# Performance work log

Hardware: AMD Instinct MI355X
Metric: run time of the kernel (lower is better)

## Reference

```python
import jax, jax.numpy as jnp
import numpy as np
from jax import lax

CHUNK = 256  # points of the query set processed per step; intermediate is [B, CHUNK, M]


def _nn_min(x, y):
    """For each point in x [B,N,3], squared distance + index of nearest point in y [B,M,3].
    Chunked over N so the full [B,N,M] distance matrix is never materialized."""
    B, N, _ = x.shape
    y2 = jnp.sum(y * y, axis=-1)  # [B, M]
    K = N // CHUNK
    xr = jnp.swapaxes(x.reshape(B, K, CHUNK, 3), 0, 1)  # [K, B, CHUNK, 3]

    def chunk_fn(xc):  # xc: [B, CHUNK, 3]
        d = (jnp.sum(xc * xc, axis=-1)[..., None]
             - 2.0 * jnp.einsum('bcd,bmd->bcm', xc, y)
             + y2[:, None, :])  # [B, CHUNK, M]
        return jnp.min(d, axis=-1), jnp.argmin(d, axis=-1).astype(jnp.int32)

    dmin, idx = lax.map(chunk_fn, xr)  # [K, B, CHUNK]
    dmin = jnp.swapaxes(dmin, 0, 1).reshape(B, N)
    idx = jnp.swapaxes(idx, 0, 1).reshape(B, N)
    return dmin, idx


def setup_inputs() -> dict:
    key = jax.random.key(0)
    k1, k2 = jax.random.split(key)
    xyz1 = jax.random.normal(k1, (8, 16384, 3), dtype=jnp.float32)
    xyz2 = jax.random.normal(k2, (8, 16384, 3), dtype=jnp.float32)
    return {"xyz1": xyz1, "xyz2": xyz2}


def reference(xyz1, xyz2):
    dist1, idx1 = _nn_min(xyz1, xyz2)  # [B, N], [B, N]
    dist2, idx2 = _nn_min(xyz2, xyz1)  # [B, M], [B, M]
    return dist1, dist2, idx1, idx2
```

## Files before the change

kernel.cpp:

```cpp
#include <hip/hip_runtime.h>
#include <stdint.h>

#define BATCH 8
#define NPTS  16384
#define BN    (BATCH * NPTS)
#define CH    256
#define NCH   (NPTS / CH)
#define QPB   256
#define MARGIN 4.0e-3f

typedef float f32x16 __attribute__((ext_vector_type(16)));
typedef short s16x8  __attribute__((ext_vector_type(8)));

__device__ __forceinline__ uint16_t bfr(float x) {
    uint32_t u = __float_as_uint(x);
    return (uint16_t)((u + 0x7FFFu + ((u >> 16) & 1u)) >> 16);
}
__device__ __forceinline__ float bff(uint16_t s) {
    return __uint_as_float(((uint32_t)s) << 16);
}
__device__ __forceinline__ void split2(float v, uint16_t* a, uint16_t* b) {
    *a = bfr(v); *b = bfr(v - bff(*a));
}
__device__ __forceinline__ uint32_t pk2(uint16_t lo, uint16_t hi) {
    return (uint32_t)lo | ((uint32_t)hi << 16);
}
__device__ __forceinline__ uint32_t key32(float d) {
    uint32_t b = __float_as_uint(d);
    return (b & 0x80000000u) ? ~b : (b | 0x80000000u);
}
__device__ __forceinline__ float dec32(uint32_t k) {
    return __uint_as_float((k & 0x80000000u) ? (k ^ 0x80000000u) : ~k);
}

#define F16(M_) M_(0) M_(1) M_(2) M_(3) M_(4) M_(5) M_(6) M_(7) \
                M_(8) M_(9) M_(10) M_(11) M_(12) M_(13) M_(14) M_(15)

#define MIN3(a, b, c) fminf(fminf((a), (b)), (c))

__device__ __forceinline__ float fold16(const f32x16 a) {
    const float u0 = MIN3(a[0],  a[1],  a[2]);
    const float u1 = MIN3(a[3],  a[4],  a[5]);
    const float u2 = MIN3(a[6],  a[7],  a[8]);
    const float u3 = MIN3(a[9],  a[10], a[11]);
    const float u4 = MIN3(a[12], a[13], a[14]);
    const float v0 = MIN3(u0, u1, a[15]);
    const float v1 = MIN3(u2, u3, u4);
    return fminf(v0, v1);
}

__global__ __launch_bounds__(256) void enc_kernel(
    const float* __restrict__ Y, uint4* __restrict__ enc,
    float4* __restrict__ y4)
{
#pragma clang fp contract(off)
    const int g = blockIdx.x * 256 + threadIdx.x;
    const int b = g >> 14, p = g & (NPTS - 1);
    const float y0 = Y[(size_t)g * 3 + 0];
    const float y1 = Y[(size_t)g * 3 + 1];
    const float y2 = Y[(size_t)g * 3 + 2];
    const float ys = (y0 * y0 + y1 * y1) + y2 * y2;
    uint16_t Ya, Yb; split2(ys, &Ya, &Yb);
    uint16_t H0, M0; split2(-2.0f * y0, &H0, &M0);
    uint16_t H1, M1; split2(-2.0f * y1, &H1, &M1);
    uint16_t H2, M2; split2(-2.0f * y2, &H2, &M2);
    const uint16_t ONE = 0x3F80;
    const int ch = p >> 8, pp = p & (CH - 1);
    const size_t base = (size_t)(b * NCH + ch) * (2 * CH) + pp;
    enc[base]      = make_uint4(pk2(ONE, ONE), pk2(Ya, Yb), pk2(H0, M0), pk2(H0, M0));
    enc[base + CH] = make_uint4(pk2(H1, M1), pk2(H1, M1), pk2(H2, M2), pk2(H2, M2));
    y4[g] = make_float4(y0, y1, y2, ys);
}

#define DECODE_DBX() \
    int dir, batch, kh, xblk; \
    { const int g = blockIdx.x; \
      if (ndir == 2) { const int s = 2 * (g & 7) + ((g >> 3) & 1); \
          dir = s >> 3; batch = s & 7; kh = (g >> 4) & 1; xblk = g >> 5; } \
      else { dir = dir0; batch = g & 7; kh = (g >> 3) & 1; xblk = g >> 4; } }

#define STAGE(c, buf) { \
        const uint4* src_ = ep + (size_t)(c) * (2 * CH); \
        _Pragma("unroll") \
        for (int i_ = 0; i_ < 2; ++i_) \
            __builtin_amdgcn_global_load_lds( \
                (const __attribute__((address_space(1))) void*)(src_ + i_ * 256 + tid), \
                (__attribute__((address_space(3))) void*)&lds[buf][i_ * 256 + tid], \
                16, 0, 0); \
    }

#define MKQFR(dst, qq, qx0v, qx1v, qx2v, qxsv) { \
        const float* xp = Xp + (size_t)(bofs + (qq)) * 3; \
        qx0v = xp[0]; qx1v = xp[1]; qx2v = xp[2]; \
        qxsv = (qx0v * qx0v + qx1v * qx1v) + qx2v * qx2v; \
        uint16_t Xa, Xb; split2(qxsv, &Xa, &Xb); \
        uint16_t h0, m0; split2(qx0v, &h0, &m0); \
        uint16_t h1, m1; split2(qx1v, &h1, &m1); \
        uint16_t h2, m2; split2(qx2v, &h2, &m2); \
        const uint16_t ONE = 0x3F80; \
        if (hi == 0) { \
            dst[0]=(short)Xa; dst[1]=(short)Xb; dst[2]=(short)ONE; dst[3]=(short)ONE; \
            dst[4]=(short)h0; dst[5]=(short)h0; dst[6]=(short)m0;  dst[7]=(short)m0; \
        } else { \
            dst[0]=(short)h1; dst[1]=(short)h1; dst[2]=(short)m1;  dst[3]=(short)m1; \
            dst[4]=(short)h2; dst[5]=(short)h2; dst[6]=(short)m2;  dst[7]=(short)m2; \
        } }

__global__ __launch_bounds__(256, 4) void nn_fused(
    const float* __restrict__ xyz1, const float* __restrict__ xyz2,
    const uint4* __restrict__ encA, const uint4* __restrict__ encB,
    const float4* __restrict__ y4A, const float4* __restrict__ y4B,
    unsigned long long* __restrict__ gkeys, int ndir, int dir0)
{
#pragma clang fp contract(off)
    __shared__ uint4 lds[2][2 * CH];
    __shared__ unsigned long long keys[QPB];

    const int tid = threadIdx.x;
    const int l   = tid & 63;
    const int wv  = tid >> 6;
    const int col = l & 31;
    const int hi  = l >> 5;
    DECODE_DBX()

    const float*  Xp = dir ? xyz2 : xyz1;
    const uint4*  ep = (dir ? encB : encA) + (size_t)batch * (NCH * 2 * CH);
    const float4* Y4 = (dir ? y4B : y4A) + (size_t)batch * NPTS;
    const int bofs  = batch * NPTS;
    const int qbase = xblk * QPB + wv * 64;
    const int chalf = NCH / 2;
    const int c0 = kh * chalf, c1 = c0 + chalf;

    keys[tid] = ~0ull;

    const f32x16 zf = {0.f,0.f,0.f,0.f,0.f,0.f,0.f,0.f,
                       0.f,0.f,0.f,0.f,0.f,0.f,0.f,0.f};

    int rowpack[4] = {0, 0, 0, 0};
    {
        s16x8 pa = {0,0,0,0,0,0,0,0}, pb = {0,0,0,0,0,0,0,0};
        if (hi == 0) { pa[0] = (short)bfr((float)col); pb[0] = (short)0x3F80; }
        const f32x16 rowp = __builtin_amdgcn_mfma_f32_32x32x16_bf16(pa, pb, zf, 0, 0, 0);
#define PR(i) rowpack[(i) >> 2] |= ((int)rowp[i] & 0xFF) << (((i) & 3) * 8);
        F16(PR)
#undef PR
    }

    s16x8 qfr0, qfr1;
    float qa0, qa1, qa2, qas, qb0, qb1, qb2, qbs;
    MKQFR(qfr0, qbase + col,      qa0, qa1, qa2, qas)
    MKQFR(qfr1, qbase + 32 + col, qb0, qb1, qb2, qbs)

    const int ldsb = hi * CH + col;

    float run0 = __builtin_inff(), run1 = __builtin_inff();

    STAGE(c0, 0);
    __syncthreads();
#pragma unroll
    for (int tp = 0; tp < CH / 32; ++tp) {
        const s16x8 pA = *(const s16x8*)&lds[0][ldsb + tp * 32];
        const f32x16 a0 = __builtin_amdgcn_mfma_f32_32x32x16_bf16(pA, qfr0, zf, 0, 0, 0);
        run0 = fminf(run0, fold16(a0));
        const f32x16 a1 = __builtin_amdgcn_mfma_f32_32x32x16_bf16(pA, qfr1, zf, 0, 0, 0);
        run1 = fminf(run1, fold16(a1));
    }
    run0 = fminf(run0, __shfl_xor(run0, 32, 64));
    run1 = fminf(run1, __shfl_xor(run1, 32, 64));

#define HITR(accv, jb, foff, thr, qx0, qx1, qx2, qxs, r) \
        if ((accv)[r] <= (thr)) { \
            const int jc = (jb) + ((rowpack[(r) >> 2] >> (((r) & 3) * 8)) & 0xFF); \
            const float4 yv = Y4[jc]; \
            const float dd = ((qxs) - 2.0f * (((qx0) * yv.x + (qx1) * yv.y) + (qx2) * yv.z)) + yv.w; \
            atomicMin(&keys[wv * 64 + (foff) + col], \
                      ((unsigned long long)key32(dd) << 32) | (uint32_t)jc); }
#define HIT(accv, jb, foff, thr, qx0, qx1, qx2, qxs) \
        { \
            HITR(accv, jb, foff, thr, qx0, qx1, qx2, qxs, 0) \
            HITR(accv, jb, foff, thr, qx0, qx1, qx2, qxs, 1) \
            HITR(accv, jb, foff, thr, qx0, qx1, qx2, qxs, 2) \
            HITR(accv, jb, foff, thr, qx0, qx1, qx2, qxs, 3) \
            HITR(accv, jb, foff, thr, qx0, qx1, qx2, qxs, 4) \
            HITR(accv, jb, foff, thr, qx0, qx1, qx2, qxs, 5) \
            HITR(accv, jb, foff, thr, qx0, qx1, qx2, qxs, 6) \
            HITR(accv, jb, foff, thr, qx0, qx1, qx2, qxs, 7) \
            HITR(accv, jb, foff, thr, qx0, qx1, qx2, qxs, 8) \
            HITR(accv, jb, foff, thr, qx0, qx1, qx2, qxs, 9) \
            HITR(accv, jb, foff, thr, qx0, qx1, qx2, qxs, 10) \
            HITR(accv, jb, foff, thr, qx0, qx1, qx2, qxs, 11) \
            HITR(accv, jb, foff, thr, qx0, qx1, qx2, qxs, 12) \
            HITR(accv, jb, foff, thr, qx0, qx1, qx2, qxs, 13) \
            HITR(accv, jb, foff, thr, qx0, qx1, qx2, qxs, 14) \
            HITR(accv, jb, foff, thr, qx0, qx1, qx2, qxs, 15) \
        }

    int cur = 0;
    for (int c = c0; c < c1; ++c) {
        if (c + 1 < c1) STAGE(c + 1, cur ^ 1);
#pragma unroll
        for (int tp = 0; tp < CH / 32; ++tp) {
            const s16x8 pA = *(const s16x8*)&lds[cur][ldsb + tp * 32];
            const int jb = c * CH + tp * 32;
            {
                const f32x16 a0 = __builtin_amdgcn_mfma_f32_32x32x16_bf16(pA, qfr0, zf, 0, 0, 0);
                const float f0 = fold16(a0);
                run0 = fminf(run0, f0);
                const float t0v = run0 + MARGIN;
                if (f0 <= t0v) HIT(a0, jb, 0, t0v, qa0, qa1, qa2, qas)
            }
            {
                const f32x16 a1 = __builtin_amdgcn_mfma_f32_32x32x16_bf16(pA, qfr1, zf, 0, 0, 0);
                const float f1 = fold16(a1);
                run1 = fminf(run1, f1);
                const float t1v = run1 + MARGIN;
                if (f1 <= t1v) HIT(a1, jb, 32, t1v, qb0, qb1, qb2, qbs)
            }
        }
        run0 = fminf(run0, __shfl_xor(run0, 32, 64));
        run1 = fminf(run1, __shfl_xor(run1, 32, 64));
        __syncthreads();
        cur ^= 1;
    }
#undef HIT
#undef HITR

    __syncthreads();
    {
        const unsigned long long m = keys[tid];
        const size_t gq = (size_t)dir * BN + bofs + (size_t)xblk * QPB + tid;
        atomicMin(&gkeys[gq], m);
    }
}

__global__ __launch_bounds__(256) void writeout_k(
    const unsigned long long* __restrict__ gkeys, float* __restrict__ out)
{
    const size_t i = (size_t)blockIdx.x * 256 + threadIdx.x;
    const unsigned long long m = gkeys[i];
    const int dir = (int)(i / BN);
    const size_t q = i - (size_t)dir * BN;
    out[(size_t)dir * BN + q]       = dec32((uint32_t)(m >> 32));
    out[(size_t)(2 + dir) * BN + q] = (float)(uint32_t)(m & 0xFFFFFFFFu);
}

extern "C" void kernel_launch(void* const* d_in, const int* in_sizes, int n_in,
                              void* d_out, int out_size, void* d_ws, size_t ws_size,
                              hipStream_t stream) {
    const float* xyz1 = (const float*)d_in[0];
    const float* xyz2 = (const float*)d_in[1];
    float* out = (float*)d_out;

    if (ws_size >= (size_t)15 * 1024 * 1024) {
        uint4*  encA = (uint4*)d_ws;
        uint4*  encB = encA + (size_t)2 * BN;
        float4* y4A  = (float4*)(encB + (size_t)2 * BN);
        float4* y4B  = y4A + BN;
        unsigned long long* gkeys = (unsigned long long*)(y4B + BN);

        enc_kernel<<<BN / 256, 256, 0, stream>>>(xyz2, encA, y4A);
        enc_kernel<<<BN / 256, 256, 0, stream>>>(xyz1, encB, y4B);
        hipMemsetAsync(gkeys, 0xFF, (size_t)2 * 1024 * 1024, stream);
        nn_fused<<<2048, 256, 0, stream>>>(xyz1, xyz2, encA, encB, y4A, y4B,
                                           gkeys, 2, 0);
        writeout_k<<<(2 * BN) / 256, 256, 0, stream>>>(gkeys, out);
    } else {
        uint4*  enc = (uint4*)d_ws;
        float4* y4  = (float4*)(enc + (size_t)2 * BN);
        unsigned long long* gkeys = (unsigned long long*)(y4 + BN);

        hipMemsetAsync(gkeys, 0xFF, (size_t)2 * 1024 * 1024, stream);
        enc_kernel<<<BN / 256, 256, 0, stream>>>(xyz2, enc, y4);
        nn_fused<<<1024, 256, 0, stream>>>(xyz1, xyz2, enc, enc, y4, y4,
                                           gkeys, 1, 0);
        enc_kernel<<<BN / 256, 256, 0, stream>>>(xyz1, enc, y4);
        nn_fused<<<1024, 256, 0, stream>>>(xyz1, xyz2, enc, enc, y4, y4,
                                           gkeys, 1, 1);
        writeout_k<<<(2 * BN) / 256, 256, 0, stream>>>(gkeys, out);
    }
}
```

Before: 413.8 us.

## Split NN search into MFMA chunk-min sweep, flagging, and exact candidate walk

Replaces the fused kernel, which checked hits inline, with a multi-pass pipeline. First an MFMA sweep records a bf16 per-chunk minimum for every query (chunk size doubled to 512) along with a global running minimum. A flag kernel then queues the chunks whose minimum lies within a margin of the best. Finally a walk kernel does exact fp32 distance evaluation over only the queued chunks, one wave per entry. This removes divergent per-element hit handling and LDS atomics from the hot MFMA loop. In exchange it adds extra launches, memsets, processes the two directions serially, tightens the margin, and caps the queue, so overflow could drop candidates.

```diff
diff --git a/kernel.cpp b/kernel.cpp
--- a/kernel.cpp
+++ b/kernel.cpp
@@ -4,10 +4,11 @@
 #define BATCH 8
 #define NPTS  16384
 #define BN    (BATCH * NPTS)
-#define CH    256
+#define CH    512
 #define NCH   (NPTS / CH)
 #define QPB   256
-#define MARGIN 4.0e-3f
+#define MARGIN 3.0e-3f
+#define QCAP  (1u << 20)
 
 typedef float f32x16 __attribute__((ext_vector_type(16)));
 typedef short s16x8  __attribute__((ext_vector_type(8)));
@@ -32,9 +33,6 @@
 __device__ __forceinline__ float dec32(uint32_t k) {
     return __uint_as_float((k & 0x80000000u) ? (k ^ 0x80000000u) : ~k);
 }
-
-#define F16(M_) M_(0) M_(1) M_(2) M_(3) M_(4) M_(5) M_(6) M_(7) \
-                M_(8) M_(9) M_(10) M_(11) M_(12) M_(13) M_(14) M_(15)
 
 #define MIN3(a, b, c) fminf(fminf((a), (b)), (c))
 
@@ -65,38 +63,31 @@
     uint16_t H1, M1; split2(-2.0f * y1, &H1, &M1);
     uint16_t H2, M2; split2(-2.0f * y2, &H2, &M2);
     const uint16_t ONE = 0x3F80;
-    const int ch = p >> 8, pp = p & (CH - 1);
+    const int ch = p >> 9, pp = p & (CH - 1);
     const size_t base = (size_t)(b * NCH + ch) * (2 * CH) + pp;
     enc[base]      = make_uint4(pk2(ONE, ONE), pk2(Ya, Yb), pk2(H0, M0), pk2(H0, M0));
     enc[base + CH] = make_uint4(pk2(H1, M1), pk2(H1, M1), pk2(H2, M2), pk2(H2, M2));
     y4[g] = make_float4(y0, y1, y2, ys);
 }
 
-#define DECODE_DBX() \
-    int dir, batch, kh, xblk; \
-    { const int g = blockIdx.x; \
-      if (ndir == 2) { const int s = 2 * (g & 7) + ((g >> 3) & 1); \
-          dir = s >> 3; batch = s & 7; kh = (g >> 4) & 1; xblk = g >> 5; } \
-      else { dir = dir0; batch = g & 7; kh = (g >> 3) & 1; xblk = g >> 4; } }
-
 #define STAGE(c, buf) { \
         const uint4* src_ = ep + (size_t)(c) * (2 * CH); \
         _Pragma("unroll") \
-        for (int i_ = 0; i_ < 2; ++i_) \
+        for (int i_ = 0; i_ < 4; ++i_) \
             __builtin_amdgcn_global_load_lds( \
                 (const __attribute__((address_space(1))) void*)(src_ + i_ * 256 + tid), \
                 (__attribute__((address_space(3))) void*)&lds[buf][i_ * 256 + tid], \
                 16, 0, 0); \
     }
 
-#define MKQFR(dst, qq, qx0v, qx1v, qx2v, qxsv) { \
-        const float* xp = Xp + (size_t)(bofs + (qq)) * 3; \
-        qx0v = xp[0]; qx1v = xp[1]; qx2v = xp[2]; \
-        qxsv = (qx0v * qx0v + qx1v * qx1v) + qx2v * qx2v; \
-        uint16_t Xa, Xb; split2(qxsv, &Xa, &Xb); \
-        uint16_t h0, m0; split2(qx0v, &h0, &m0); \
-        uint16_t h1, m1; split2(qx1v, &h1, &m1); \
-        uint16_t h2, m2; split2(qx2v, &h2, &m2); \
+#define MKQFR(dst, qq) { \
+        const float* xp = Xp + (size_t)(qq) * 3; \
+        const float x0 = xp[0], x1 = xp[1], x2 = xp[2]; \
+        const float xs = (x0 * x0 + x1 * x1) + x2 * x2; \
+        uint16_t Xa, Xb; split2(xs, &Xa, &Xb); \
+        uint16_t h0, m0; split2(x0, &h0, &m0); \
+        uint16_t h1, m1; split2(x1, &h1, &m1); \
+        uint16_t h2, m2; split2(x2, &h2, &m2); \
         const uint16_t ONE = 0x3F80; \
         if (hi == 0) { \
             dst[0]=(short)Xa; dst[1]=(short)Xb; dst[2]=(short)ONE; dst[3]=(short)ONE; \
@@ -106,140 +97,146 @@
             dst[4]=(short)h2; dst[5]=(short)h2; dst[6]=(short)m2;  dst[7]=(short)m2; \
         } }
 
-__global__ __launch_bounds__(256, 4) void nn_fused(
-    const float* __restrict__ xyz1, const float* __restrict__ xyz2,
-    const uint4* __restrict__ encA, const uint4* __restrict__ encB,
-    const float4* __restrict__ y4A, const float4* __restrict__ y4B,
-    unsigned long long* __restrict__ gkeys, int ndir, int dir0)
+__global__ __launch_bounds__(256, 4) void nn_sweep1(
+    const float* __restrict__ Xp, const uint4* __restrict__ encp,
+    uint32_t* __restrict__ mkey, uint16_t* __restrict__ cmin16)
 {
 #pragma clang fp contract(off)
     __shared__ uint4 lds[2][2 * CH];
-    __shared__ unsigned long long keys[QPB];
 
     const int tid = threadIdx.x;
     const int l   = tid & 63;
     const int wv  = tid >> 6;
     const int col = l & 31;
     const int hi  = l >> 5;
-    DECODE_DBX()
-
-    const float*  Xp = dir ? xyz2 : xyz1;
-    const uint4*  ep = (dir ? encB : encA) + (size_t)batch * (NCH * 2 * CH);
-    const float4* Y4 = (dir ? y4B : y4A) + (size_t)batch * NPTS;
+
+    const int g     = blockIdx.x;
+    const int batch = g & 7;
+    const int kh    = (g >> 3) & 1;
+    const int xblk  = g >> 4;
+
+    const uint4* ep = encp + (size_t)batch * (NCH * 2 * CH);
     const int bofs  = batch * NPTS;
-    const int qbase = xblk * QPB + wv * 64;
-    const int chalf = NCH / 2;
-    const int c0 = kh * chalf, c1 = c0 + chalf;
-
-    keys[tid] = ~0ull;
+    const int qbase = bofs + xblk * QPB + wv * 64;
+    const int c0 = kh * (NCH / 2), c1 = c0 + NCH / 2;
 
     const f32x16 zf = {0.f,0.f,0.f,0.f,0.f,0.f,0.f,0.f,
                        0.f,0.f,0.f,0.f,0.f,0.f,0.f,0.f};
 
-    int rowpack[4] = {0, 0, 0, 0};
-    {
-        s16x8 pa = {0,0,0,0,0,0,0,0}, pb = {0,0,0,0,0,0,0,0};
-        if (hi == 0) { pa[0] = (short)bfr((float)col); pb[0] = (short)0x3F80; }
-        const f32x16 rowp = __builtin_amdgcn_mfma_f32_32x32x16_bf16(pa, pb, zf, 0, 0, 0);
-#define PR(i) rowpack[(i) >> 2] |= ((int)rowp[i] & 0xFF) << (((i) & 3) * 8);
-        F16(PR)
-#undef PR
-    }
-
     s16x8 qfr0, qfr1;
-    float qa0, qa1, qa2, qas, qb0, qb1, qb2, qbs;
-    MKQFR(qfr0, qbase + col,      qa0, qa1, qa2, qas)
-    MKQFR(qfr1, qbase + 32 + col, qb0, qb1, qb2, qbs)
+    MKQFR(qfr0, qbase + col)
+    MKQFR(qfr1, qbase + 32 + col)
 
     const int ldsb = hi * CH + col;
 
     float run0 = __builtin_inff(), run1 = __builtin_inff();
-
     STAGE(c0, 0);
     __syncthreads();
-#pragma unroll
-    for (int tp = 0; tp < CH / 32; ++tp) {
-        const s16x8 pA = *(const s16x8*)&lds[0][ldsb + tp * 32];
-        const f32x16 a0 = __builtin_amdgcn_mfma_f32_32x32x16_bf16(pA, qfr0, zf, 0, 0, 0);
-        run0 = fminf(run0, fold16(a0));
-        const f32x16 a1 = __builtin_amdgcn_mfma_f32_32x32x16_bf16(pA, qfr1, zf, 0, 0, 0);
-        run1 = fminf(run1, fold16(a1));
-    }
-    run0 = fminf(run0, __shfl_xor(run0, 32, 64));
-    run1 = fminf(run1, __shfl_xor(run1, 32, 64));
-
-#define HITR(accv, jb, foff, thr, qx0, qx1, qx2, qxs, r) \
-        if ((accv)[r] <= (thr)) { \
-            const int jc = (jb) + ((rowpack[(r) >> 2] >> (((r) & 3) * 8)) & 0xFF); \
-            const float4 yv = Y4[jc]; \
-            const float dd = ((qxs) - 2.0f * (((qx0) * yv.x + (qx1) * yv.y) + (qx2) * yv.z)) + yv.w; \
-            atomicMin(&keys[wv * 64 + (foff) + col], \
-                      ((unsigned long long)key32(dd) << 32) | (uint32_t)jc); }
-#define HIT(accv, jb, foff, thr, qx0, qx1, qx2, qxs) \
-        { \
-            HITR(accv, jb, foff, thr, qx0, qx1, qx2, qxs, 0) \
-            HITR(accv, jb, foff, thr, qx0, qx1, qx2, qxs, 1) \
-            HITR(accv, jb, foff, thr, qx0, qx1, qx2, qxs, 2) \
-            HITR(accv, jb, foff, thr, qx0, qx1, qx2, qxs, 3) \
-            HITR(accv, jb, foff, thr, qx0, qx1, qx2, qxs, 4) \
-            HITR(accv, jb, foff, thr, qx0, qx1, qx2, qxs, 5) \
-            HITR(accv, jb, foff, thr, qx0, qx1, qx2, qxs, 6) \
-            HITR(accv, jb, foff, thr, qx0, qx1, qx2, qxs, 7) \
-            HITR(accv, jb, foff, thr, qx0, qx1, qx2, qxs, 8) \
-            HITR(accv, jb, foff, thr, qx0, qx1, qx2, qxs, 9) \
-            HITR(accv, jb, foff, thr, qx0, qx1, qx2, qxs, 10) \
-            HITR(accv, jb, foff, thr, qx0, qx1, qx2, qxs, 11) \
-            HITR(accv, jb, foff, thr, qx0, qx1, qx2, qxs, 12) \
-            HITR(accv, jb, foff, thr, qx0, qx1, qx2, qxs, 13) \
-            HITR(accv, jb, foff, thr, qx0, qx1, qx2, qxs, 14) \
-            HITR(accv, jb, foff, thr, qx0, qx1, qx2, qxs, 15) \
-        }
-
     int cur = 0;
     for (int c = c0; c < c1; ++c) {
         if (c + 1 < c1) STAGE(c + 1, cur ^ 1);
+        float cm0 = __builtin_inff(), cm1 = __builtin_inff();
 #pragma unroll
         for (int tp = 0; tp < CH / 32; ++tp) {
             const s16x8 pA = *(const s16x8*)&lds[cur][ldsb + tp * 32];
-            const int jb = c * CH + tp * 32;
-            {
-                const f32x16 a0 = __builtin_amdgcn_mfma_f32_32x32x16_bf16(pA, qfr0, zf, 0, 0, 0);
-                const float f0 = fold16(a0);
-                run0 = fminf(run0, f0);
-                const float t0v = run0 + MARGIN;
-                if (f0 <= t0v) HIT(a0, jb, 0, t0v, qa0, qa1, qa2, qas)
-            }
-            {
-                const f32x16 a1 = __builtin_amdgcn_mfma_f32_32x32x16_bf16(pA, qfr1, zf, 0, 0, 0);
-                const float f1 = fold16(a1);
-                run1 = fminf(run1, f1);
-                const float t1v = run1 + MARGIN;
-                if (f1 <= t1v) HIT(a1, jb, 32, t1v, qb0, qb1, qb2, qbs)
-            }
-        }
-        run0 = fminf(run0, __shfl_xor(run0, 32, 64));
-        run1 = fminf(run1, __shfl_xor(run1, 32, 64));
+            const f32x16 a0 = __builtin_amdgcn_mfma_f32_32x32x16_bf16(pA, qfr0, zf, 0, 0, 0);
+            cm0 = fminf(cm0, fold16(a0));
+            const f32x16 a1 = __builtin_amdgcn_mfma_f32_32x32x16_bf16(pA, qfr1, zf, 0, 0, 0);
+            cm1 = fminf(cm1, fold16(a1));
+        }
+        cm0 = fminf(cm0, __shfl_xor(cm0, 32, 64));
+        cm1 = fminf(cm1, __shfl_xor(cm1, 32, 64));
+        run0 = fminf(run0, cm0);
+        run1 = fminf(run1, cm1);
+        if (l < 32) {
+            cmin16[(size_t)(qbase + col) * NCH + c]      =
+                (uint16_t)(__float_as_uint(cm0) >> 16);
+            cmin16[(size_t)(qbase + 32 + col) * NCH + c] =
+                (uint16_t)(__float_as_uint(cm1) >> 16);
+        }
         __syncthreads();
         cur ^= 1;
     }
-#undef HIT
-#undef HITR
-
-    __syncthreads();
-    {
-        const unsigned long long m = keys[tid];
-        const size_t gq = (size_t)dir * BN + bofs + (size_t)xblk * QPB + tid;
-        atomicMin(&gkeys[gq], m);
+    if (l < 32) {
+        atomicMin(&mkey[qbase + col],      key32(run0));
+        atomicMin(&mkey[qbase + 32 + col], key32(run1));
+    }
+}
+
+__global__ __launch_bounds__(256) void flag_kernel(
+    const uint32_t* __restrict__ mkey, const uint16_t* __restrict__ cmin16,
+    uint32_t* __restrict__ queue, uint32_t* __restrict__ qcount)
+{
+    const int q = blockIdx.x * 256 + threadIdx.x;
+    const float thr = dec32(mkey[q]) + MARGIN + 1.0e-5f;
+    const uint4* row = (const uint4*)(cmin16 + (size_t)q * NCH);
+    uint32_t fl = 0;
+#pragma unroll
+    for (int w = 0; w < 4; ++w) {
+        const uint4 u = row[w];
+        const uint32_t c[4] = {u.x, u.y, u.z, u.w};
+#pragma unroll
+        for (int j = 0; j < 4; ++j) {
+            if (bff((uint16_t)(c[j] & 0xFFFF)) <= thr) fl |= 1u << (w * 8 + j * 2);
+            if (bff((uint16_t)(c[j] >> 16))    <= thr) fl |= 1u << (w * 8 + j * 2 + 1);
+        }
+    }
+    const int nfl = __popc(fl);
+    uint32_t base = atomicAdd(qcount, (uint32_t)nfl);
+    while (fl) {
+        const int ch = __ffs(fl) - 1;
+        fl &= fl - 1;
+        if (base < QCAP) queue[base] = ((uint32_t)q << 5) | (uint32_t)ch;
+        ++base;
+    }
+}
+
+__global__ __launch_bounds__(256, 8) void walk_kernel(
+    const float* __restrict__ Xp, const float4* __restrict__ y4,
+    const uint32_t* __restrict__ queue, const uint32_t* __restrict__ qcount,
+    unsigned long long* __restrict__ gkeys)
+{
+#pragma clang fp contract(off)
+    const int lane = threadIdx.x & 63;
+    const uint32_t wid = blockIdx.x * 4 + (threadIdx.x >> 6);
+    const uint32_t nw  = gridDim.x * 4;
+    const uint32_t cnt = min(*qcount, QCAP);
+
+    for (uint32_t e = wid; e < cnt; e += nw) {
+        const uint32_t entry = queue[e];
+        const int q  = (int)(entry >> 5);
+        const int ch = (int)(entry & 31);
+        const int b  = q >> 14;
+
+        const float* xp = Xp + (size_t)q * 3;
+        const float qx0 = xp[0], qx1 = xp[1], qx2 = xp[2];
+        const float qxs = (qx0 * qx0 + qx1 * qx1) + qx2 * qx2;
+
+        const float4* yb = y4 + (size_t)b * NPTS + (size_t)ch * CH;
+        unsigned long long best = ~0ull;
+#pragma unroll
+        for (int j = 0; j < CH / 64; ++j) {
+            const int k = j * 64 + lane;
+            const float4 yv = yb[k];
+            const float dd = (qxs - 2.0f * ((qx0 * yv.x + qx1 * yv.y) + qx2 * yv.z)) + yv.w;
+            const unsigned long long key =
+                ((unsigned long long)key32(dd) << 32) | (uint32_t)(ch * CH + k);
+            if (key < best) best = key;
+        }
+#pragma unroll
+        for (int m = 1; m <= 32; m <<= 1) {
+            const unsigned long long o = __shfl_xor(best, m, 64);
+            if (o < best) best = o;
+        }
+        if (lane == 0) atomicMin(&gkeys[q], best);
     }
 }
 
 __global__ __launch_bounds__(256) void writeout_k(
-    const unsigned long long* __restrict__ gkeys, float* __restrict__ out)
-{
-    const size_t i = (size_t)blockIdx.x * 256 + threadIdx.x;
-    const unsigned long long m = gkeys[i];
-    const int dir = (int)(i / BN);
-    const size_t q = i - (size_t)dir * BN;
+    const unsigned long long* __restrict__ gkeys, float* __restrict__ out, int dir)
+{
+    const size_t q = (size_t)blockIdx.x * 256 + threadIdx.x;
+    const unsigned long long m = gkeys[q];
     out[(size_t)dir * BN + q]       = dec32((uint32_t)(m >> 32));
     out[(size_t)(2 + dir) * BN + q] = (float)(uint32_t)(m & 0xFFFFFFFFu);
 }
@@ -251,31 +248,28 @@
     const float* xyz2 = (const float*)d_in[1];
     float* out = (float*)d_out;
 
-    if (ws_size >= (size_t)15 * 1024 * 1024) {
-        uint4*  encA = (uint4*)d_ws;
-        uint4*  encB = encA + (size_t)2 * BN;
-        float4* y4A  = (float4*)(encB + (size_t)2 * BN);
-        float4* y4B  = y4A + BN;
-        unsigned long long* gkeys = (unsigned long long*)(y4B + BN);
-
-        enc_kernel<<<BN / 256, 256, 0, stream>>>(xyz2, encA, y4A);
-        enc_kernel<<<BN / 256, 256, 0, stream>>>(xyz1, encB, y4B);
-        hipMemsetAsync(gkeys, 0xFF, (size_t)2 * 1024 * 1024, stream);
-        nn_fused<<<2048, 256, 0, stream>>>(xyz1, xyz2, encA, encB, y4A, y4B,
-                                           gkeys, 2, 0);
-        writeout_k<<<(2 * BN) / 256, 256, 0, stream>>>(gkeys, out);
-    } else {
-        uint4*  enc = (uint4*)d_ws;
-        float4* y4  = (float4*)(enc + (size_t)2 * BN);
-        unsigned long long* gkeys = (unsigned long long*)(y4 + BN);
-
-        hipMemsetAsync(gkeys, 0xFF, (size_t)2 * 1024 * 1024, stream);
-        enc_kernel<<<BN / 256, 256, 0, stream>>>(xyz2, enc, y4);
-        nn_fused<<<1024, 256, 0, stream>>>(xyz1, xyz2, enc, enc, y4, y4,
-                                           gkeys, 1, 0);
-        enc_kernel<<<BN / 256, 256, 0, stream>>>(xyz1, enc, y4);
-        nn_fused<<<1024, 256, 0, stream>>>(xyz1, xyz2, enc, enc, y4, y4,
-                                           gkeys, 1, 1);
-        writeout_k<<<(2 * BN) / 256, 256, 0, stream>>>(gkeys, out);
-    }
-}
+    char* base = (char*)d_ws;
+    uint4*    enc    = (uint4*)base;
+    uint32_t* queue  = (uint32_t*)base;
+    float4*   y4     = (float4*)(base + (size_t)4 * 1024 * 1024);
+    uint32_t* mkey   = (uint32_t*)(base + (size_t)6 * 1024 * 1024);
+    uint16_t* cmin16 = (uint16_t*)(base + (size_t)6 * 1024 * 1024 + 512 * 1024);
+    unsigned long long* gkeys =
+        (unsigned long long*)(base + (size_t)14 * 1024 * 1024 + 512 * 1024);
+    uint32_t* qcount = (uint32_t*)(base + (size_t)15 * 1024 * 1024 + 512 * 1024);
+
+    for (int dir = 0; dir < 2; ++dir) {
+        const float* Xq = dir ? xyz2 : xyz1;
+        const float* Yp = dir ? xyz1 : xyz2;
+
+        hipMemsetAsync(mkey, 0xFF, (size_t)BN * 4, stream);
+        hipMemsetAsync(gkeys, 0xFF, (size_t)BN * 8, stream);
+        hipMemsetAsync(qcount, 0, 256, stream);
+
+        enc_kernel<<<BN / 256, 256, 0, stream>>>(Yp, enc, y4);
+        nn_sweep1<<<1024, 256, 0, stream>>>(Xq, enc, mkey, cmin16);
+        flag_kernel<<<BN / 256, 256, 0, stream>>>(mkey, cmin16, queue, qcount);
+        walk_kernel<<<2048, 256, 0, stream>>>(Xq, y4, queue, qcount, gkeys);
+        writeout_k<<<BN / 256, 256, 0, stream>>>(gkeys, out, dir);
+    }
+}
```

New measurement: 408.6 us. No clear change (-1.2%).
